# Performance work log

Hardware: AMD Instinct MI355X
Metric: run time of the kernel (lower is better)

Reference implementation:

```python
import jax, jax.numpy as jnp
import numpy as np

KS = 7            # kernel_size
DIL = 1           # dilatation
H = 96
W = 96
PAD = DIL * (KS - 1) // 2
SHIFTS = [s * DIL for s in range(KS)]


def stack_kernel(a, axis=-2):
    # a: [B, H+2*PAD, W+2*PAD, C] -> [B, H, W, ks^2, C] (or stacked on `axis`)
    return jnp.stack([a[:, y:H + y, x:W + x] for y in SHIFTS for x in SHIFTS], axis=axis)


def make_padding_mask():
    # zeros inside, -inf in the halo; stacked per window position -> [1,H,W,ks^2]
    z = jnp.pad(jnp.zeros((1, H, W, 1), jnp.float32),
                ((0, 0), (PAD, PAD), (PAD, PAD), (0, 0)),
                constant_values=-jnp.inf)
    return stack_kernel(z, axis=-1)[..., 0, :]  # [1,H,W,ks^2]


def setup_inputs() -> dict:
    key = jax.random.key(0)
    ks = jax.random.split(key, 8)
    B, C, KD, OD = 2, 128, 64, 128
    Q = jax.random.normal(ks[0], (B, H, W, C), jnp.float32)
    K = jax.random.normal(ks[1], (B, H, W, C), jnp.float32)
    V = jax.random.normal(ks[2], (B, H, W, C), jnp.float32)
    s = 1.0 / np.sqrt(C)
    Wq = jax.random.normal(ks[3], (C, KD), jnp.float32) * s
    Wk = jax.random.normal(ks[4], (C, KD), jnp.float32) * s
    Wv = jax.random.normal(ks[5], (C, OD), jnp.float32) * s
    return {"Q": Q, "K": K, "V": V,
            "Wq": Wq, "bq": jnp.zeros((KD,), jnp.float32),
            "Wk": Wk, "bk": jnp.zeros((KD,), jnp.float32),
            "Wv": Wv, "bv": jnp.zeros((OD,), jnp.float32)}


def reference(Q, K, V, Wq, bq, Wk, bk, Wv, bv):
    # Dense projections (key_dim is not None)
    q = Q @ Wq + bq                      # [B,H,W,KD]
    k = K @ Wk + bk                      # [B,H,W,KD]
    Dk = jnp.asarray(q.shape[-1], q.dtype)

    pad4 = ((0, 0), (PAD, PAD), (PAD, PAD), (0, 0))
    k_stk = stack_kernel(jnp.pad(k, pad4), axis=-2)   # [B,H,W,ks^2,KD]
    mask = make_padding_mask()                        # [1,H,W,ks^2]

    # w = Q . K_neighbors + padding mask; softmax over ks^2 window
    w = jnp.einsum('bhwd,bhwkd->bhwk', q, k_stk) + mask
    scores = jax.nn.softmax(w / jnp.sqrt(Dk), axis=-1)  # [B,H,W,ks^2]

    v_stk = stack_kernel(jnp.pad(V, pad4), axis=-2)   # [B,H,W,ks^2,E]
    out = jnp.einsum('bhwk,bhwke->bhwe', scores, v_stk)
    # V_d Dense with relu (out_dim is not None)
    out = jax.nn.relu(out @ Wv + bv)                  # [B,H,W,out_dim]
    return out
```

## Files before the change

kernel.cpp:

```cpp
#include <hip/hip_runtime.h>
#include <math.h>

#define BH 2
#define HH 96
#define WW 96
#define NPIX (BH*HH*WW)

#define TH 8
#define TW 4
#define NH 140
#define NHP 160

#define NEGBIG (-3.0e38f)

typedef __attribute__((ext_vector_type(8))) short short8;
typedef __attribute__((ext_vector_type(4))) float f32x4;

__device__ __forceinline__ unsigned short f2bf(float f) {
    union { float f; unsigned u; } a; a.f = f;
    return (unsigned short)((a.u + 0x7FFFu + ((a.u >> 16) & 1u)) >> 16);
}
__device__ __forceinline__ unsigned packbf(float x, float y) {
    return (unsigned)f2bf(x) | ((unsigned)f2bf(y) << 16);
}

#define WT_STRIDE 136

__global__ __launch_bounds__(256) void prep_proj_kernel(
    const float* __restrict__ Qg, const float* __restrict__ Kg,
    const float* __restrict__ V,  const float* __restrict__ Wq,
    const float* __restrict__ bq, const float* __restrict__ Wk,
    const float* __restrict__ bk, const float* __restrict__ Wv,
    unsigned short* __restrict__ q_bf, unsigned short* __restrict__ k_bf,
    unsigned short* __restrict__ v_bf, unsigned short* __restrict__ WvT)
{
    __shared__ unsigned short WT[64 * WT_STRIDE];
    const int bid = blockIdx.x;
    const int tid = threadIdx.x;

    if (bid < 576) {
        const bool isq = bid < 288;
        const float* __restrict__ X   = isq ? Qg : Kg;
        const float* __restrict__ Wt  = isq ? Wq : Wk;
        const float* __restrict__ bia = isq ? bq : bk;
        unsigned short* __restrict__ Y = isq ? q_bf : k_bf;

        {
            const float4* __restrict__ W4 = reinterpret_cast<const float4*>(Wt);
            #pragma unroll
            for (int i = 0; i < 8; ++i) {
                const int e  = tid + 256 * i;
                const int k  = e >> 4;
                const int n4 = (e & 15) * 4;
                const float4 v = W4[e];
                WT[(n4 + 0) * WT_STRIDE + k] = f2bf(v.x);
                WT[(n4 + 1) * WT_STRIDE + k] = f2bf(v.y);
                WT[(n4 + 2) * WT_STRIDE + k] = f2bf(v.z);
                WT[(n4 + 3) * WT_STRIDE + k] = f2bf(v.w);
            }
        }
        __syncthreads();

        const int lane = tid & 63;
        const int wvv  = tid >> 6;
        const int row0 = ((bid % 288) * 4 + wvv) * 16;
        const int qd = lane >> 4, m = lane & 15;

        short8 afr[4];
        #pragma unroll
        for (int ks = 0; ks < 4; ++ks) {
            const float4* __restrict__ src = reinterpret_cast<const float4*>(
                X + (size_t)(row0 + m) * 128 + ks * 32 + qd * 8);
            const float4 a0 = src[0], a1 = src[1];
            short8 f;
            f[0] = (short)f2bf(a0.x); f[1] = (short)f2bf(a0.y);
            f[2] = (short)f2bf(a0.z); f[3] = (short)f2bf(a0.w);
            f[4] = (short)f2bf(a1.x); f[5] = (short)f2bf(a1.y);
            f[6] = (short)f2bf(a1.z); f[7] = (short)f2bf(a1.w);
            afr[ks] = f;
        }

        #pragma unroll
        for (int n = 0; n < 4; ++n) {
            f32x4 acc = {};
            #pragma unroll
            for (int ks = 0; ks < 4; ++ks) {
                const short8 bfr = *reinterpret_cast<const short8*>(
                    &WT[(n * 16 + m) * WT_STRIDE + ks * 32 + qd * 8]);
                acc = __builtin_amdgcn_mfma_f32_16x16x32_bf16(afr[ks], bfr, acc, 0, 0, 0);
            }
            const int col = n * 16 + m;
            const float bb = bia[col];
            #pragma unroll
            for (int r = 0; r < 4; ++r)
                Y[(size_t)(row0 + qd * 4 + r) * 64 + col] = f2bf(acc[r] + bb);
        }
    } else if (bid < 1728) {
        const int idx = (bid - 576) * 256 + tid;
        const float4* __restrict__ V4 = reinterpret_cast<const float4*>(V);
        const float4 a = V4[idx * 2], b = V4[idx * 2 + 1];
        uint4 o;
        o.x = packbf(a.x, a.y); o.y = packbf(a.z, a.w);
        o.z = packbf(b.x, b.y); o.w = packbf(b.z, b.w);
        reinterpret_cast<uint4*>(v_bf)[idx] = o;
    } else {
        const int base = (bid - 1728) * 1024 + tid * 4;
        #pragma unroll
        for (int i = 0; i < 4; ++i) {
            const int e = base + i;
            WvT[e] = f2bf(Wv[(e & 127) * 128 + (e >> 7)]);
        }
    }
}

#define PS_OFF 0
#define PS_STRIDE 168
#define AS_OFF 5376
#define AS_STRIDE 136
#define SM_OFF 9728
#define OFF_OFF 10240
#define LDS_N 10560

__global__ __launch_bounds__(512) void attn_kernel(
    const unsigned short* __restrict__ q_bf, const unsigned short* __restrict__ k_bf,
    const unsigned short* __restrict__ v_bf, const unsigned short* __restrict__ WvT,
    const float* __restrict__ bv, float* __restrict__ out)
{
    __shared__ unsigned short lds[LDS_N];
    const int tid  = threadIdx.x;
    const int lane = tid & 63;
    const int wv   = tid >> 6;
    const int mt   = wv & 1;
    const int ng   = wv >> 1;

    const int bid  = blockIdx.x;
    const int bimg = bid / 288;
    const int tidx = bid % 288;
    const int ty = tidx / 24, tx = tidx % 24;
    const int y0 = ty * TH, x0 = tx * TW;

    const int qd = lane >> 4, m = lane & 15;

    int*   __restrict__ offsI = reinterpret_cast<int*>(&lds[OFF_OFF]);
    float* __restrict__ smf   = reinterpret_cast<float*>(&lds[SM_OFF]);

    if (tid < NHP) {
        const int r = tid;
        const int hy = (r * 6554) >> 16;
        const int hx = r - hy * 10;
        const int iy = y0 - 3 + hy, ix = x0 - 3 + hx;
        int o = -1;
        if (((unsigned)iy < HH) & ((unsigned)ix < WW) & (r < NH))
            o = (bimg * HH + iy) * WW + ix;
        offsI[r] = o;
    }

    short8 qa[2];
    {
        const int py = mt * 4 + (m >> 2), px = m & 3;
        const size_t gq = (size_t)(bimg * HH + y0 + py) * WW + (x0 + px);
        #pragma unroll
        for (int ks = 0; ks < 2; ++ks)
            qa[ks] = *reinterpret_cast<const short8*>(q_bf + gq * 64 + ks * 32 + qd * 8);
    }

    const int ntbase = (ng < 2) ? ng * 3 : 6 + (ng - 2) * 2;
    const int ntcnt  = (ng < 2) ? 3 : 2;

    f32x4 sc[3];
    #pragma unroll
    for (int n5 = 0; n5 < 3; ++n5) {
        if (n5 >= ntcnt) break;
        const int h  = (ntbase + n5) * 16 + m;
        const int hy = (h * 6554) >> 16;
        const int hx = h - hy * 10;
        const int iy = y0 - 3 + hy, ix = x0 - 3 + hx;
        const bool ok = ((unsigned)iy < HH) & ((unsigned)ix < WW) & (h < NH);
        const size_t ob = ok ? (size_t)((bimg * HH + iy) * WW + ix) * 64 : 0;
        f32x4 a = {};
        #pragma unroll
        for (int ks = 0; ks < 2; ++ks) {
            const short8 bfr = *reinterpret_cast<const short8*>(k_bf + ob + ks * 32 + qd * 8);
            a = __builtin_amdgcn_mfma_f32_16x16x32_bf16(qa[ks], bfr, a, 0, 0, 0);
        }
        sc[n5] = a;
    }

    float mx[4] = {NEGBIG, NEGBIG, NEGBIG, NEGBIG};
    #pragma unroll
    for (int n5 = 0; n5 < 3; ++n5) {
        if (n5 >= ntcnt) break;
        const int h  = (ntbase + n5) * 16 + m;
        const int hy = (h * 6554) >> 16;
        const int hx = h - hy * 10;
        const int iy = y0 - 3 + hy, ix = x0 - 3 + hx;
        const bool imgok = ((unsigned)iy < HH) & ((unsigned)ix < WW) & (h < NH);
        const int py = mt * 4 + qd;
        #pragma unroll
        for (int r = 0; r < 4; ++r) {
            const bool ok = imgok & ((unsigned)(hy - py) <= 6u) & ((unsigned)(hx - r) <= 6u);
            const float s = ok ? sc[n5][r] * 0.125f : NEGBIG;
            sc[n5][r] = s;
            mx[r] = fmaxf(mx[r], s);
        }
    }
    #pragma unroll
    for (int r = 0; r < 4; ++r)
        #pragma unroll
        for (int off = 1; off < 16; off <<= 1)
            mx[r] = fmaxf(mx[r], __shfl_xor(mx[r], off));

    float sm[4] = {0.f, 0.f, 0.f, 0.f};
    #pragma unroll
    for (int n5 = 0; n5 < 3; ++n5) {
        if (n5 >= ntcnt) break;
        #pragma unroll
        for (int r = 0; r < 4; ++r) {
            const float s = sc[n5][r];
            const float e = (s > -1.0e38f) ? __expf(s - mx[r]) : 0.f;
            sc[n5][r] = e;
            sm[r] += e;
        }
    }
    #pragma unroll
    for (int r = 0; r < 4; ++r)
        #pragma unroll
        for (int off = 1; off < 16; off <<= 1)
            sm[r] += __shfl_xor(sm[r], off);

    if (m == 0) {
        #pragma unroll
        for (int r = 0; r < 4; ++r) {
            const int row = mt * 16 + qd * 4 + r;
            smf[row * 4 + ng]       = mx[r];
            smf[128 + row * 4 + ng] = sm[r];
        }
    }
    __syncthreads();

    float fac[4];
    #pragma unroll
    for (int r = 0; r < 4; ++r) {
        const int row = mt * 16 + qd * 4 + r;
        float M = smf[row * 4 + 0];
        M = fmaxf(M, smf[row * 4 + 1]);
        M = fmaxf(M, smf[row * 4 + 2]);
        M = fmaxf(M, smf[row * 4 + 3]);
        float S = 0.f;
        #pragma unroll
        for (int g = 0; g < 4; ++g) {
            const float mg = smf[row * 4 + g];
            const float eg = (mg > -1.0e38f) ? __expf(mg - M) : 0.f;
            S += smf[128 + row * 4 + g] * eg;
        }
        const float eo = (mx[r] > -1.0e38f) ? __expf(mx[r] - M) : 0.f;
        fac[r] = eo / S;
    }

    #pragma unroll
    for (int n5 = 0; n5 < 3; ++n5) {
        if (n5 >= ntcnt) break;
        #pragma unroll
        for (int r = 0; r < 4; ++r) {
            const int row = mt * 16 + qd * 4 + r;
            const int col = (ntbase + n5) * 16 + m;
            lds[PS_OFF + row * PS_STRIDE + col] = f2bf(sc[n5][r] * fac[r]);
        }
    }
    __syncthreads();

    short8 pa[5];
    #pragma unroll
    for (int ks = 0; ks < 5; ++ks)
        pa[ks] = *reinterpret_cast<const short8*>(
            &lds[PS_OFF + (mt * 16 + m) * PS_STRIDE + ks * 32 + qd * 8]);

    f32x4 oacc[2] = {};
    #pragma unroll
    for (int ks = 0; ks < 5; ++ks) {
        const int kbase = ks * 32 + qd * 8;
        const unsigned short* vb[8];
        #pragma unroll
        for (int j = 0; j < 8; ++j) {
            const int o = offsI[kbase + j];
            vb[j] = v_bf + (size_t)(o < 0 ? 0 : o) * 128;
        }
        #pragma unroll
        for (int n2 = 0; n2 < 2; ++n2) {
            const int ch = (ng * 2 + n2) * 16 + m;
            short8 bfr;
            #pragma unroll
            for (int j = 0; j < 8; ++j)
                bfr[j] = (short)vb[j][ch];
            oacc[n2] = __builtin_amdgcn_mfma_f32_16x16x32_bf16(pa[ks], bfr, oacc[n2], 0, 0, 0);
        }
    }

    #pragma unroll
    for (int n2 = 0; n2 < 2; ++n2)
        #pragma unroll
        for (int r = 0; r < 4; ++r) {
            const int row = mt * 16 + qd * 4 + r;
            const int col = (ng * 2 + n2) * 16 + m;
            lds[AS_OFF + row * AS_STRIDE + col] = f2bf(oacc[n2][r]);
        }
    __syncthreads();

    short8 aa[4];
    #pragma unroll
    for (int ks = 0; ks < 4; ++ks)
        aa[ks] = *reinterpret_cast<const short8*>(
            &lds[AS_OFF + (mt * 16 + m) * AS_STRIDE + ks * 32 + qd * 8]);

    #pragma unroll
    for (int n2 = 0; n2 < 2; ++n2) {
        const int nt = ng * 2 + n2;
        f32x4 a = {};
        #pragma unroll
        for (int ks = 0; ks < 4; ++ks) {
            const short8 bfr = *reinterpret_cast<const short8*>(
                WvT + (nt * 16 + m) * 128 + ks * 32 + qd * 8);
            a = __builtin_amdgcn_mfma_f32_16x16x32_bf16(aa[ks], bfr, a, 0, 0, 0);
        }
        const int col = nt * 16 + m;
        const float bb = bv[col];
        #pragma unroll
        for (int r = 0; r < 4; ++r) {
            const int py = mt * 4 + qd, px = r;
            const size_t gp = (size_t)(bimg * HH + y0 + py) * WW + (x0 + px);
            out[gp * 128 + col] = fmaxf(a[r] + bb, 0.f);
        }
    }
}

extern "C" void kernel_launch(void* const* d_in, const int* in_sizes, int n_in,
                              void* d_out, int out_size, void* d_ws, size_t ws_size,
                              hipStream_t stream)
{
    const float* Q  = (const float*)d_in[0];
    const float* K  = (const float*)d_in[1];
    const float* V  = (const float*)d_in[2];
    const float* Wq = (const float*)d_in[3];
    const float* bq = (const float*)d_in[4];
    const float* Wk = (const float*)d_in[5];
    const float* bk = (const float*)d_in[6];
    const float* Wv = (const float*)d_in[7];
    const float* bv = (const float*)d_in[8];
    float* out = (float*)d_out;

    unsigned short* wbase = (unsigned short*)d_ws;
    unsigned short* WvT   = wbase + 16384;
    unsigned short* q_bf  = wbase + 32768;
    unsigned short* k_bf  = q_bf + (size_t)NPIX * 64;
    unsigned short* v_bf  = k_bf + (size_t)NPIX * 64;

    prep_proj_kernel<<<1744, 256, 0, stream>>>(Q, K, V, Wq, bq, Wk, bk, Wv,
                                               q_bf, k_bf, v_bf, WvT);
    attn_kernel<<<576, 512, 0, stream>>>(q_bf, k_bf, v_bf, WvT, bv, out);
}
```

Baseline: 109.8 us.

## Stage V halo tile in LDS as transposed bf16 inside attention kernel

Result: slower. 116.7 us (+6.3%).

```diff
diff --git a/kernel.cpp b/kernel.cpp
--- a/kernel.cpp
+++ b/kernel.cpp
@@ -9,7 +9,6 @@
 #define TH 8
 #define TW 4
 #define NH 140
-#define NHP 160
 
 #define NEGBIG (-3.0e38f)
 
@@ -20,19 +19,16 @@
     union { float f; unsigned u; } a; a.f = f;
     return (unsigned short)((a.u + 0x7FFFu + ((a.u >> 16) & 1u)) >> 16);
 }
-__device__ __forceinline__ unsigned packbf(float x, float y) {
-    return (unsigned)f2bf(x) | ((unsigned)f2bf(y) << 16);
-}
 
 #define WT_STRIDE 136
 
 __global__ __launch_bounds__(256) void prep_proj_kernel(
     const float* __restrict__ Qg, const float* __restrict__ Kg,
-    const float* __restrict__ V,  const float* __restrict__ Wq,
-    const float* __restrict__ bq, const float* __restrict__ Wk,
-    const float* __restrict__ bk, const float* __restrict__ Wv,
+    const float* __restrict__ Wq, const float* __restrict__ bq,
+    const float* __restrict__ Wk, const float* __restrict__ bk,
+    const float* __restrict__ Wv,
     unsigned short* __restrict__ q_bf, unsigned short* __restrict__ k_bf,
-    unsigned short* __restrict__ v_bf, unsigned short* __restrict__ WvT)
+    unsigned short* __restrict__ WvT)
 {
     __shared__ unsigned short WT[64 * WT_STRIDE];
     const int bid = blockIdx.x;
@@ -95,16 +91,8 @@
             for (int r = 0; r < 4; ++r)
                 Y[(size_t)(row0 + qd * 4 + r) * 64 + col] = f2bf(acc[r] + bb);
         }
-    } else if (bid < 1728) {
-        const int idx = (bid - 576) * 256 + tid;
-        const float4* __restrict__ V4 = reinterpret_cast<const float4*>(V);
-        const float4 a = V4[idx * 2], b = V4[idx * 2 + 1];
-        uint4 o;
-        o.x = packbf(a.x, a.y); o.y = packbf(a.z, a.w);
-        o.z = packbf(b.x, b.y); o.w = packbf(b.z, b.w);
-        reinterpret_cast<uint4*>(v_bf)[idx] = o;
     } else {
-        const int base = (bid - 1728) * 1024 + tid * 4;
+        const int base = (bid - 576) * 1024 + tid * 4;
         #pragma unroll
         for (int i = 0; i < 4; ++i) {
             const int e = base + i;
@@ -118,12 +106,13 @@
 #define AS_OFF 5376
 #define AS_STRIDE 136
 #define SM_OFF 9728
-#define OFF_OFF 10240
-#define LDS_N 10560
+#define V_OFF 10240
+#define VS 168
+#define LDS_N 31744
 
 __global__ __launch_bounds__(512) void attn_kernel(
     const unsigned short* __restrict__ q_bf, const unsigned short* __restrict__ k_bf,
-    const unsigned short* __restrict__ v_bf, const unsigned short* __restrict__ WvT,
+    const float* __restrict__ V, const unsigned short* __restrict__ WvT,
     const float* __restrict__ bv, float* __restrict__ out)
 {
     __shared__ unsigned short lds[LDS_N];
@@ -141,18 +130,27 @@
 
     const int qd = lane >> 4, m = lane & 15;
 
-    int*   __restrict__ offsI = reinterpret_cast<int*>(&lds[OFF_OFF]);
-    float* __restrict__ smf   = reinterpret_cast<float*>(&lds[SM_OFF]);
-
-    if (tid < NHP) {
-        const int r = tid;
-        const int hy = (r * 6554) >> 16;
-        const int hx = r - hy * 10;
-        const int iy = y0 - 3 + hy, ix = x0 - 3 + hx;
-        int o = -1;
-        if (((unsigned)iy < HH) & ((unsigned)ix < WW) & (r < NH))
-            o = (bimg * HH + iy) * WW + ix;
-        offsI[r] = o;
+    float* __restrict__ smf = reinterpret_cast<float*>(&lds[SM_OFF]);
+
+    {
+        const int p0 = tid >> 4;
+        const int g  = tid & 15;
+        #pragma unroll
+        for (int rnd = 0; rnd < 5; ++rnd) {
+            const int p  = rnd * 32 + p0;
+            const int hy = (p * 6554) >> 16;
+            const int hx = p - hy * 10;
+            const int iy = y0 - 3 + hy, ix = x0 - 3 + hx;
+            const bool ok = ((unsigned)iy < HH) & ((unsigned)ix < WW) & (p < NH);
+            const size_t o = ok ? (size_t)((bimg * HH + iy) * WW + ix) : 0;
+            const float4* __restrict__ s4 = reinterpret_cast<const float4*>(V + o * 128 + g * 8);
+            const float4 a = s4[0], b = s4[1];
+            unsigned short* __restrict__ dst = &lds[V_OFF + (g * 8) * VS + p];
+            dst[0 * VS] = f2bf(a.x); dst[1 * VS] = f2bf(a.y);
+            dst[2 * VS] = f2bf(a.z); dst[3 * VS] = f2bf(a.w);
+            dst[4 * VS] = f2bf(b.x); dst[5 * VS] = f2bf(b.y);
+            dst[6 * VS] = f2bf(b.z); dst[7 * VS] = f2bf(b.w);
+        }
     }
 
     short8 qa[2];
@@ -279,19 +277,11 @@
     #pragma unroll
     for (int ks = 0; ks < 5; ++ks) {
         const int kbase = ks * 32 + qd * 8;
-        const unsigned short* vb[8];
-        #pragma unroll
-        for (int j = 0; j < 8; ++j) {
-            const int o = offsI[kbase + j];
-            vb[j] = v_bf + (size_t)(o < 0 ? 0 : o) * 128;
-        }
         #pragma unroll
         for (int n2 = 0; n2 < 2; ++n2) {
             const int ch = (ng * 2 + n2) * 16 + m;
-            short8 bfr;
-            #pragma unroll
-            for (int j = 0; j < 8; ++j)
-                bfr[j] = (short)vb[j][ch];
+            const short8 bfr = *reinterpret_cast<const short8*>(
+                &lds[V_OFF + ch * VS + kbase]);
             oacc[n2] = __builtin_amdgcn_mfma_f32_16x16x32_bf16(pa[ks], bfr, oacc[n2], 0, 0, 0);
         }
     }
@@ -352,9 +342,8 @@
     unsigned short* WvT   = wbase + 16384;
     unsigned short* q_bf  = wbase + 32768;
     unsigned short* k_bf  = q_bf + (size_t)NPIX * 64;
-    unsigned short* v_bf  = k_bf + (size_t)NPIX * 64;
-
-    prep_proj_kernel<<<1744, 256, 0, stream>>>(Q, K, V, Wq, bq, Wk, bk, Wv,
-                                               q_bf, k_bf, v_bf, WvT);
-    attn_kernel<<<576, 512, 0, stream>>>(q_bf, k_bf, v_bf, WvT, bv, out);
+
+    prep_proj_kernel<<<592, 256, 0, stream>>>(Q, K, Wq, bq, Wk, bk, Wv,
+                                              q_bf, k_bf, WvT);
+    attn_kernel<<<576, 512, 0, stream>>>(q_bf, k_bf, V, WvT, bv, out);
 }
```
